# Kernel optimization log

Hardware: AMD Instinct MI355X
Metric: run time of the kernel (lower is better)

## Reference

```python
import jax, jax.numpy as jnp
import numpy as np

NUM_HEADS = 16


def setup_inputs() -> dict:
    key = jax.random.key(0)
    kx, kp, kq, kw, kb = jax.random.split(key, 5)
    B, N, C = 2, 2048, 1024
    x = jax.random.normal(kx, (B, N, C), dtype=jnp.float32)
    padding_mask = jax.random.randint(kp, (B, N), 0, 2).astype(jnp.bool_)
    W_qkv = jax.random.normal(kq, (C, 3 * C), dtype=jnp.float32) * (C ** -0.5)
    W_proj = jax.random.normal(kw, (C, C), dtype=jnp.float32) * (C ** -0.5)
    b_proj = jax.random.normal(kb, (C,), dtype=jnp.float32) * 0.02
    return {"x": x, "padding_mask": padding_mask, "causal_start": 128,
            "W_qkv": W_qkv, "W_proj": W_proj, "b_proj": b_proj}


def reference(x, padding_mask, causal_start, W_qkv, W_proj, b_proj):
    B, N, C = x.shape
    H = NUM_HEADS
    d = C // H
    scale = d ** -0.5
    # qkv projection: (B,N,3C) -> (3,B,H,N,d)
    qkv = (x @ W_qkv).reshape(B, N, 3, H, d).transpose(2, 0, 3, 1, 4)
    q, k, v = qkv[0], qkv[1], qkv[2]
    attn = jnp.einsum("bhqd,bhkd->bhqk", q * scale, k)  # (B,H,N,N)
    # padding mask: mask out padded KEY positions
    attn = jnp.where(padding_mask[:, None, None, :], -jnp.inf, attn)
    # offset causal mask: lower-triangular, but first `causal_start` columns always visible
    allowed = jnp.tril(jnp.ones((N, N), dtype=jnp.bool_))
    allowed = allowed | (jnp.arange(N)[None, :] < causal_start)
    attn = jnp.where(~allowed[None, None, :, :], -jnp.inf, attn)
    attn = jax.nn.softmax(attn.astype(jnp.float32), axis=-1).astype(x.dtype)
    out = jnp.einsum("bhqk,bhkd->bhqd", attn, v)  # (B,H,N,d)
    out = out.transpose(0, 2, 1, 3).reshape(B, N, C)
    return out @ W_proj + b_proj
```

## Files before the change

### kernel.cpp

```cpp
#include <hip/hip_runtime.h>
#include <stdint.h>

typedef unsigned short ushort_t;
typedef __attribute__((ext_vector_type(4))) unsigned short ushort4_t;
typedef __attribute__((ext_vector_type(8))) short short8;
typedef __attribute__((ext_vector_type(4))) float float4_t;

#define AS1 __attribute__((address_space(1)))
#define AS3 __attribute__((address_space(3)))

__device__ inline ushort_t f2bf(float f) {
    unsigned x = __builtin_bit_cast(unsigned, f);
    unsigned r = x + 0x7fffu + ((x >> 16) & 1u);
    return (ushort_t)(r >> 16);
}
__device__ inline ushort_t f2bf_trunc(float f) {
    return (ushort_t)(__builtin_bit_cast(unsigned, f) >> 16);
}

__global__ __launch_bounds__(256) void prep_fused(
    const float* __restrict__ wqkv, const float* __restrict__ x,
    const int* __restrict__ pad,
    ushort_t* __restrict__ wqkvT, ushort_t* __restrict__ xbf,
    int* __restrict__ tbl) {
    __shared__ __align__(16) ushort_t tile[64][65];
    __shared__ int wsum[4];
    int bid = blockIdx.x, t = threadIdx.x;
    if (bid < 768) {
        int bx = bid % 48, by = bid / 48;
        int c0 = bx * 64, r0 = by * 64;
        for (int i = 0; i < 16; i++) {
            int idx = t + i * 256;
            int lr = idx >> 6, lc = idx & 63;
            tile[lr][lc] = f2bf(wqkv[(size_t)(r0 + lr) * 3072 + c0 + lc]);
        }
        __syncthreads();
        for (int i = 0; i < 16; i++) {
            int idx = t + i * 256;
            int lr = idx >> 6, lc = idx & 63;
            wqkvT[(size_t)(c0 + lr) * 1024 + r0 + lc] = tile[lc][lr];
        }
    } else if (bid < 2816) {
        size_t i = ((size_t)(bid - 768) * 256 + t) * 8;
        float4_t a = *(const float4_t*)(x + i);
        float4_t b = *(const float4_t*)(x + i + 4);
        ushort_t u[8];
        u[0] = f2bf(a.x); u[1] = f2bf(a.y); u[2] = f2bf(a.z); u[3] = f2bf(a.w);
        u[4] = f2bf(b.x); u[5] = f2bf(b.y); u[6] = f2bf(b.z); u[7] = f2bf(b.w);
        *(ushort4_t*)(xbf + i) = *(ushort4_t*)&u[0];
        *(ushort4_t*)(xbf + i + 4) = *(ushort4_t*)&u[4];
    } else {
        int b = bid - 2816;
        int* cvtab = tbl;
        int* pref = tbl + 4096;
        int* idxmap = tbl + 8192;
        int* vcp = tbl + 12288;
        int lane = t & 63, w4 = t >> 6;
        int base0 = t * 8;
        int v[8], s8 = 0;
        for (int j = 0; j < 8; j++) {
            v[j] = (pad[b * 2048 + base0 + j] == 0) ? 1 : 0;
            s8 += v[j];
        }
        int incl = s8;
        for (int off = 1; off < 64; off <<= 1) {
            int y = __shfl_up(incl, off, 64);
            if (lane >= off) incl += y;
        }
        int excl = incl - s8;
        if (lane == 63) wsum[w4] = incl;
        __syncthreads();
        int wbase = 0;
        for (int ww = 0; ww < 4; ww++) if (ww < w4) wbase += wsum[ww];
        int vcall = wsum[0] + wsum[1] + wsum[2] + wsum[3];
        int run = wbase + excl;
        for (int j = 0; j < 8; j++) {
            int pos = base0 + j;
            pref[b * 2048 + pos] = run;
            cvtab[b * 2048 + pos] = v[j] ? run : -1;
            if (v[j]) idxmap[b * 2048 + run] = pos;
            run += v[j];
        }
        if (t == 0) vcp[b] = vcall;
        for (int s = vcall + t; s < 2048; s += 256) idxmap[b * 2048 + s] = 2048;
    }
}

__global__ __launch_bounds__(256) void transpose_f32_bf16(const float* __restrict__ in,
                                                          ushort_t* __restrict__ out,
                                                          int R, int C) {
    __shared__ __align__(16) ushort_t tile[64][65];
    int c0 = blockIdx.x * 64, r0 = blockIdx.y * 64;
    int t = threadIdx.x;
    for (int i = 0; i < 16; i++) {
        int idx = t + i * 256;
        int lr = idx >> 6, lc = idx & 63;
        tile[lr][lc] = f2bf(in[(size_t)(r0 + lr) * C + c0 + lc]);
    }
    __syncthreads();
    for (int i = 0; i < 16; i++) {
        int idx = t + i * 256;
        int lr = idx >> 6, lc = idx & 63;
        out[(size_t)(c0 + lr) * R + r0 + lc] = tile[lc][lr];
    }
}

__global__ __launch_bounds__(256) void gemm_qkv(
    const ushort_t* __restrict__ A, const ushort_t* __restrict__ Bt,
    const int* __restrict__ cvtab,
    ushort_t* __restrict__ outQ, ushort_t* __restrict__ outK, ushort_t* __restrict__ outV) {
    const int K = 1024;
    __shared__ __align__(16) ushort_t As[128 * 64];
    __shared__ __align__(16) ushort_t Bs[128 * 64];
    int t = threadIdx.x;
    int w = t >> 6, lane = t & 63;
    int quad = lane >> 4, l15 = lane & 15;
    int wM = w >> 1, wN = w & 1;
    int tM = blockIdx.y * 128, tN = blockIdx.x * 128;

    float4_t acc[4][4];
    for (int i = 0; i < 4; i++)
        for (int j = 0; j < 4; j++) acc[i][j] = (float4_t){0.f, 0.f, 0.f, 0.f};

    int lrow = lane >> 3;
    int lcol8 = (lane & 7) * 8;

    const ushort_t* Abase = A + (size_t)(tM + w * 32) * K;
    const ushort_t* Bbase = Bt + (size_t)(tN + w * 32) * K;

    for (int k0 = 0; k0 < K; k0 += 64) {
        __syncthreads();
        for (int i = 0; i < 4; i++) {
            const ushort_t* ga = Abase + (size_t)(i * 8 + lrow) * K + k0 + lcol8;
            __builtin_amdgcn_global_load_lds((AS1 void*)ga, (AS3 void*)&As[(w * 32 + i * 8) * 64], 16, 0, 0);
            const ushort_t* gb = Bbase + (size_t)(i * 8 + lrow) * K + k0 + lcol8;
            __builtin_amdgcn_global_load_lds((AS1 void*)gb, (AS3 void*)&Bs[(w * 32 + i * 8) * 64], 16, 0, 0);
        }
        __syncthreads();
        for (int kt = 0; kt < 2; kt++) {
            short8 af[4], bf[4];
            for (int m = 0; m < 4; m++)
                af[m] = *(const short8*)&As[(wM * 64 + m * 16 + l15) * 64 + kt * 32 + quad * 8];
            for (int n = 0; n < 4; n++)
                bf[n] = *(const short8*)&Bs[(wN * 64 + n * 16 + l15) * 64 + kt * 32 + quad * 8];
            for (int m = 0; m < 4; m++)
                for (int n = 0; n < 4; n++)
                    acc[m][n] = __builtin_amdgcn_mfma_f32_16x16x32_bf16(af[m], bf[n], acc[m][n], 0, 0, 0);
        }
    }

    for (int m = 0; m < 4; m++) {
        int gm = tM + wM * 64 + m * 16 + quad * 4;
        int cvv[4];
        for (int r = 0; r < 4; r++) cvv[r] = cvtab[gm + r];
        for (int n = 0; n < 4; n++) {
            int gn = tN + wN * 64 + n * 16 + l15;
            int three = gn >> 10;
            int h = (gn >> 6) & 15;
            int dd = gn & 63;
            for (int r = 0; r < 4; r++) {
                int row = gm + r;
                int b = row >> 11;
                ushort_t val = f2bf(acc[m][n][r]);
                if (three == 0) {
                    int ns = row & 2047;
                    outQ[(((size_t)(b * 16 + h) * 2048 + ns) << 6) + dd] = val;
                } else {
                    int slot = cvv[r];
                    if (slot >= 0) {
                        ushort_t* dst = (three == 1) ? outK : outV;
                        dst[(((size_t)(b * 16 + h) * 2048 + slot) << 6) + dd] = val;
                    }
                }
            }
        }
    }
}

__global__ __launch_bounds__(512, 4) void attn_kernel(
    const ushort_t* __restrict__ q, const ushort_t* __restrict__ k,
    const ushort_t* __restrict__ v, const int* __restrict__ tbl,
    const int* __restrict__ csp, ushort_t* __restrict__ out) {
    __shared__ __align__(16) ushort_t Ks[2][64 * 64];
    __shared__ __align__(16) ushort_t VsT[2][64 * 64];
    __shared__ __align__(16) ushort_t Ps[8][16 * 64];
    __shared__ int Idx[2048];

    const int* pref = tbl + 4096;
    const int* idxmap = tbl + 8192;
    const int* vcp = tbl + 12288;

    int cs = csp[0];
    int t = threadIdx.x, w = t >> 6, lane = t & 63;
    int quad = lane >> 4, l15 = lane & 15;
    int bh = blockIdx.y;
    int b = bh >> 4, h = bh & 15;
    int g = (blockIdx.y < 16) ? blockIdx.x : 15 - blockIdx.x;
    int q0 = g * 128;
    int rowmin = q0 + w * 16;
    const float c1 = 0.18033688f;
    const float c2 = -11.541560f;

    int bound = q0 + 128; if (cs > bound) bound = cs;
    int nvalid = (bound > 2047) ? vcp[b] : pref[b * 2048 + bound];
    int nT = (nvalid + 63) >> 6; if (nT < 1) nT = 1;

    for (int i = 0; i < 4; i++) Idx[t + i * 512] = idxmap[b * 2048 + t + i * 512];

    const ushort_t* qb = q + ((size_t)bh * 2048 + rowmin + l15) * 64;
    short8 qf0 = *(const short8*)(qb + quad * 8);
    short8 qf1 = *(const short8*)(qb + 32 + quad * 8);

    float4_t O[4];
    for (int i = 0; i < 4; i++) O[i] = (float4_t){0.f, 0.f, 0.f, 0.f};
    float ls[4] = {0.f, 0.f, 0.f, 0.f};

    const ushort_t* kbase = k + (size_t)bh * 2048 * 64;
    const ushort_t* vbase = v + (size_t)bh * 2048 * 64;

    int lrow = lane >> 3, lblk = lane & 7;
    int prow = rowmin + quad * 4;
    int sw = l15 & 7;

    short8 vr;
    auto stageK = [&](int it, int buf) {
        int k0 = it * 64;
        const ushort_t* gk = kbase + (size_t)(k0 + w * 8 + lrow) * 64 + ((lblk ^ lrow) * 8);
        __builtin_amdgcn_global_load_lds((AS1 void*)gk, (AS3 void*)&Ks[buf][w * 8 * 64], 16, 0, 0);
    };
    auto loadV = [&](int it) {
        vr = *(const short8*)(vbase + (size_t)(it * 64 + lane) * 64 + w * 8);
        if (it * 64 + lane >= nvalid)
            for (int j = 0; j < 8; j++) vr[j] = 0;
    };

    stageK(0, 0);
    loadV(0);

    for (int it = 0; it < nT; it++) {
        int cur = it & 1, nxt = cur ^ 1;
        for (int j = 0; j < 8; j++) {
            int sl = ((lrow ^ j) * 8) + lblk;
            VsT[cur][(w * 8 + j) * 64 + sl] = (ushort_t)vr[j];
        }
        __syncthreads();
        if (it + 1 < nT) {
            stageK(it + 1, nxt);
            loadV(it + 1);
        }

        int k0 = it * 64;
        int omin = Idx[k0];
        bool act = (omin <= rowmin + 15) || (omin < cs);
        if (act) {
            int omax = Idx[k0 + 63];
            bool needC = (omax > rowmin) && (omax >= cs);

            short8 kf0[4], kf1[4];
            for (int ks = 0; ks < 4; ks++) {
                const ushort_t* krow = &Ks[cur][(ks * 16 + l15) * 64];
                kf0[ks] = *(const short8*)(krow + (quad ^ sw) * 8);
                kf1[ks] = *(const short8*)(krow + ((4 + quad) ^ sw) * 8);
            }

            float4_t s[4];
            for (int ks = 0; ks < 4; ks++) {
                float4_t a = (float4_t){0.f, 0.f, 0.f, 0.f};
                a = __builtin_amdgcn_mfma_f32_16x16x32_bf16(qf0, kf0[ks], a, 0, 0, 0);
                a = __builtin_amdgcn_mfma_f32_16x16x32_bf16(qf1, kf1[ks], a, 0, 0, 0);
                s[ks] = a;
            }
            for (int ks = 0; ks < 4; ks++) {
                int key = Idx[k0 + ks * 16 + l15];
                for (int r = 0; r < 4; r++) {
                    float arg = s[ks][r] * c1 + c2;
                    if (needC && (key > prow + r) && (key >= cs)) arg = -1e38f;
                    float p = __builtin_amdgcn_exp2f(arg);
                    ls[r] += p;
                    int row = quad * 4 + r;
                    Ps[w][row * 64 + (((ks * 2 + (l15 >> 3)) ^ (row & 7)) * 8) + (l15 & 7)] = f2bf_trunc(p);
                }
            }

            short8 vf0[4], vf1[4];
            for (int n = 0; n < 4; n++) {
                const ushort_t* vrow = &VsT[cur][(n * 16 + l15) * 64];
                vf0[n] = *(const short8*)(vrow + (quad ^ sw) * 8);
                vf1[n] = *(const short8*)(vrow + ((4 + quad) ^ sw) * 8);
            }
            const ushort_t* prl = &Ps[w][l15 * 64];
            short8 pf0 = *(const short8*)(prl + (quad ^ sw) * 8);
            short8 pf1 = *(const short8*)(prl + ((4 + quad) ^ sw) * 8);
            for (int n = 0; n < 4; n++) {
                O[n] = __builtin_amdgcn_mfma_f32_16x16x32_bf16(pf0, vf0[n], O[n], 0, 0, 0);
                O[n] = __builtin_amdgcn_mfma_f32_16x16x32_bf16(pf1, vf1[n], O[n], 0, 0, 0);
            }
        }
    }

    for (int r = 0; r < 4; r++) {
        float l = ls[r];
        l += __shfl_xor(l, 1, 64); l += __shfl_xor(l, 2, 64);
        l += __shfl_xor(l, 4, 64); l += __shfl_xor(l, 8, 64);
        float inv = l > 0.f ? 1.f / l : 0.f;
        int row = rowmin + quad * 4 + r;
        size_t ob = ((size_t)b * 2048 + row) * 1024 + h * 64;
        for (int n = 0; n < 4; n++)
            out[ob + n * 16 + l15] = f2bf(O[n][r] * inv);
    }
}

__global__ __launch_bounds__(256) void gemm_out_k(
    const ushort_t* __restrict__ A, const ushort_t* __restrict__ Bt,
    const float* __restrict__ bias, float* __restrict__ outC) {
    const int K = 1024, N = 1024;
    __shared__ __align__(16) ushort_t As[128 * 64];
    __shared__ __align__(16) ushort_t Bs[128 * 64];
    int t = threadIdx.x;
    int w = t >> 6, lane = t & 63;
    int quad = lane >> 4, l15 = lane & 15;
    int wM = w >> 1, wN = w & 1;
    int tM = blockIdx.y * 128, tN = blockIdx.x * 128;

    float4_t acc[4][4];
    for (int i = 0; i < 4; i++)
        for (int j = 0; j < 4; j++) acc[i][j] = (float4_t){0.f, 0.f, 0.f, 0.f};

    int lrow = lane >> 3;
    int lcol8 = (lane & 7) * 8;

    const ushort_t* Abase = A + (size_t)(tM + w * 32) * K;
    const ushort_t* Bbase = Bt + (size_t)(tN + w * 32) * K;

    for (int k0 = 0; k0 < K; k0 += 64) {
        __syncthreads();
        for (int i = 0; i < 4; i++) {
            const ushort_t* ga = Abase + (size_t)(i * 8 + lrow) * K + k0 + lcol8;
            __builtin_amdgcn_global_load_lds((AS1 void*)ga, (AS3 void*)&As[(w * 32 + i * 8) * 64], 16, 0, 0);
            const ushort_t* gb = Bbase + (size_t)(i * 8 + lrow) * K + k0 + lcol8;
            __builtin_amdgcn_global_load_lds((AS1 void*)gb, (AS3 void*)&Bs[(w * 32 + i * 8) * 64], 16, 0, 0);
        }
        __syncthreads();
        for (int kt = 0; kt < 2; kt++) {
            short8 af[4], bf[4];
            for (int m = 0; m < 4; m++)
                af[m] = *(const short8*)&As[(wM * 64 + m * 16 + l15) * 64 + kt * 32 + quad * 8];
            for (int n = 0; n < 4; n++)
                bf[n] = *(const short8*)&Bs[(wN * 64 + n * 16 + l15) * 64 + kt * 32 + quad * 8];
            for (int m = 0; m < 4; m++)
                for (int n = 0; n < 4; n++)
                    acc[m][n] = __builtin_amdgcn_mfma_f32_16x16x32_bf16(af[m], bf[n], acc[m][n], 0, 0, 0);
        }
    }

    for (int m = 0; m < 4; m++) {
        int gm = tM + wM * 64 + m * 16 + quad * 4;
        for (int n = 0; n < 4; n++) {
            int gn = tN + wN * 64 + n * 16 + l15;
            float bv = bias[gn];
            for (int r = 0; r < 4; r++)
                outC[(size_t)(gm + r) * N + gn] = acc[m][n][r] + bv;
        }
    }
}

extern "C" void kernel_launch(void* const* d_in, const int* in_sizes, int n_in,
                              void* d_out, int out_size, void* d_ws, size_t ws_size,
                              hipStream_t stream) {
    const float* x = (const float*)d_in[0];
    const int* pad = (const int*)d_in[1];
    const int* cs = (const int*)d_in[2];
    const float* wqkv = (const float*)d_in[3];
    const float* wproj = (const float*)d_in[4];
    const float* bproj = (const float*)d_in[5];
    float* out = (float*)d_out;

    ushort_t* ws = (ushort_t*)d_ws;
    ushort_t* qws = ws;
    ushort_t* kws = ws + (size_t)4194304;
    ushort_t* vws = ws + (size_t)8388608;
    ushort_t* wqkvT = ws + (size_t)12582912;
    ushort_t* aows = ws + (size_t)12582912;
    ushort_t* wprojT = ws;
    ushort_t* xbf = (ushort_t*)d_out;
    int* tbl = (int*)((char*)d_out + 8388608);

    prep_fused<<<2818, 256, 0, stream>>>(wqkv, x, pad, wqkvT, xbf, tbl);
    gemm_qkv<<<dim3(24, 32), 256, 0, stream>>>(xbf, wqkvT, tbl, qws, kws, vws);
    attn_kernel<<<dim3(16, 32), 512, 0, stream>>>(qws, kws, vws, tbl, cs, aows);
    transpose_f32_bf16<<<dim3(16, 16), 256, 0, stream>>>(wproj, wprojT, 1024, 1024);
    gemm_out_k<<<dim3(8, 32), 256, 0, stream>>>(aows, wprojT, bproj, out);
}
```

Baseline: 200.1 us.

## Compute K/V projection only for unpadded rows via gathered A rows

Splits the QKV GEMM grid into Q blocks and K/V blocks. K/V blocks gather A rows through the compacted index map and exit early for tiles beyond the valid key count. Masked keys were previously computed and then discarded, so this removes roughly half of the K/V GEMM work. The cost is indirect row addressing on the A loads and a grid-shape dependency that the launch side must match.

```diff
diff --git a/kernel.cpp b/kernel.cpp
--- a/kernel.cpp
+++ b/kernel.cpp
@@ -107,31 +107,51 @@
 
 __global__ __launch_bounds__(256) void gemm_qkv(
     const ushort_t* __restrict__ A, const ushort_t* __restrict__ Bt,
-    const int* __restrict__ cvtab,
+    const int* __restrict__ tbl,
     ushort_t* __restrict__ outQ, ushort_t* __restrict__ outK, ushort_t* __restrict__ outV) {
     const int K = 1024;
     __shared__ __align__(16) ushort_t As[128 * 64];
     __shared__ __align__(16) ushort_t Bs[128 * 64];
+    const int* idxmap = tbl + 8192;
+    const int* vcp = tbl + 12288;
     int t = threadIdx.x;
     int w = t >> 6, lane = t & 63;
     int quad = lane >> 4, l15 = lane & 15;
     int wM = w >> 1, wN = w & 1;
-    int tM = blockIdx.y * 128, tN = blockIdx.x * 128;
+    int lrow = lane >> 3;
+    int lcol8 = (lane & 7) * 8;
+
+    bool isQ = blockIdx.x < 8;
+    int b = 0, m0, vc = 0, tNr;
+    size_t arow[4];
+    if (isQ) {
+        tNr = blockIdx.x * 128;
+        m0 = blockIdx.y * 128;
+        for (int i = 0; i < 4; i++)
+            arow[i] = (size_t)(m0 + w * 32 + i * 8 + lrow) * K;
+    } else {
+        tNr = 1024 + (blockIdx.x - 8) * 128;
+        b = blockIdx.y >> 4;
+        vc = vcp[b];
+        m0 = (blockIdx.y & 15) * 128;
+        if (m0 >= vc) return;
+        for (int i = 0; i < 4; i++) {
+            int slot = m0 + w * 32 + i * 8 + lrow;
+            int orig = idxmap[b * 2048 + slot];
+            arow[i] = (size_t)(b * 2048 + orig) * K;
+        }
+    }
 
     float4_t acc[4][4];
     for (int i = 0; i < 4; i++)
         for (int j = 0; j < 4; j++) acc[i][j] = (float4_t){0.f, 0.f, 0.f, 0.f};
 
-    int lrow = lane >> 3;
-    int lcol8 = (lane & 7) * 8;
-
-    const ushort_t* Abase = A + (size_t)(tM + w * 32) * K;
-    const ushort_t* Bbase = Bt + (size_t)(tN + w * 32) * K;
+    const ushort_t* Bbase = Bt + (size_t)(tNr + w * 32) * K;
 
     for (int k0 = 0; k0 < K; k0 += 64) {
         __syncthreads();
         for (int i = 0; i < 4; i++) {
-            const ushort_t* ga = Abase + (size_t)(i * 8 + lrow) * K + k0 + lcol8;
+            const ushort_t* ga = A + arow[i] + k0 + lcol8;
             __builtin_amdgcn_global_load_lds((AS1 void*)ga, (AS3 void*)&As[(w * 32 + i * 8) * 64], 16, 0, 0);
             const ushort_t* gb = Bbase + (size_t)(i * 8 + lrow) * K + k0 + lcol8;
             __builtin_amdgcn_global_load_lds((AS1 void*)gb, (AS3 void*)&Bs[(w * 32 + i * 8) * 64], 16, 0, 0);
@@ -150,27 +170,25 @@
     }
 
     for (int m = 0; m < 4; m++) {
-        int gm = tM + wM * 64 + m * 16 + quad * 4;
-        int cvv[4];
-        for (int r = 0; r < 4; r++) cvv[r] = cvtab[gm + r];
+        int lm = wM * 64 + m * 16 + quad * 4;
         for (int n = 0; n < 4; n++) {
-            int gn = tN + wN * 64 + n * 16 + l15;
-            int three = gn >> 10;
-            int h = (gn >> 6) & 15;
-            int dd = gn & 63;
-            for (int r = 0; r < 4; r++) {
-                int row = gm + r;
-                int b = row >> 11;
-                ushort_t val = f2bf(acc[m][n][r]);
-                if (three == 0) {
-                    int ns = row & 2047;
-                    outQ[(((size_t)(b * 16 + h) * 2048 + ns) << 6) + dd] = val;
-                } else {
-                    int slot = cvv[r];
-                    if (slot >= 0) {
-                        ushort_t* dst = (three == 1) ? outK : outV;
-                        dst[(((size_t)(b * 16 + h) * 2048 + slot) << 6) + dd] = val;
-                    }
+            int lnc = wN * 64 + n * 16 + l15;
+            if (isQ) {
+                int gn = tNr + lnc;
+                int h = gn >> 6, dd = gn & 63;
+                for (int r = 0; r < 4; r++) {
+                    int row = m0 + lm + r;
+                    int bb = row >> 11, ns = row & 2047;
+                    outQ[(((size_t)(bb * 16 + h) * 2048 + ns) << 6) + dd] = f2bf(acc[m][n][r]);
+                }
+            } else {
+                int gnc = tNr - 1024 + lnc;
+                ushort_t* dst = (gnc < 1024) ? outK : outV;
+                int hh = (gnc >> 6) & 15, dd = gnc & 63;
+                for (int r = 0; r < 4; r++) {
+                    int slot = m0 + lm + r;
+                    if (slot < vc)
+                        dst[(((size_t)(b * 16 + hh) * 2048 + slot) << 6) + dd] = f2bf(acc[m][n][r]);
                 }
             }
         }
```

After: 191.0 us. -4.5%, faster.
